# Performance work log

Measured on AMD Instinct MI355X. Metric: run time of the kernel, lower is better.

Reference implementation:

```python
import jax, jax.numpy as jnp
import numpy as np

HIDDEN = 2048
N_HEADS = 16
N_KV_HEADS = 4
HEAD_DIM = HIDDEN // N_HEADS  # 128
N_GROUPS = N_HEADS // N_KV_HEADS  # 4
ROPE_BASE = 10000.0


def rope_cos_sin(seq_len, dim, dtype=jnp.float32):
    inv_freq = 1.0 / (ROPE_BASE ** (jnp.arange(0, dim, 2, dtype=jnp.float32) / dim))
    t = jnp.arange(seq_len, dtype=jnp.float32)
    freqs = jnp.einsum('i,j->ij', t, inv_freq)          # [S, dim/2]
    emb = jnp.concatenate([freqs, freqs], axis=-1)       # [S, dim]
    return emb.astype(dtype).cos(), emb.astype(dtype).sin() if False else (jnp.cos(emb).astype(dtype), jnp.sin(emb).astype(dtype))[1] and None or (jnp.cos(emb).astype(dtype), jnp.sin(emb).astype(dtype))


def _rope_tables(seq_len, dim):
    inv_freq = 1.0 / (ROPE_BASE ** (jnp.arange(0, dim, 2, dtype=jnp.float32) / dim))
    t = jnp.arange(seq_len, dtype=jnp.float32)
    freqs = jnp.einsum('i,j->ij', t, inv_freq)
    emb = jnp.concatenate([freqs, freqs], axis=-1)
    return jnp.cos(emb), jnp.sin(emb)  # each [S, dim]


def rotate_half(x):
    d = x.shape[-1] // 2
    return jnp.concatenate([-x[..., d:], x[..., :d]], axis=-1)


def setup_inputs() -> dict:
    key = jax.random.key(0)
    ks = jax.random.split(key, 5)
    B, S = 2, 2048
    std = 0.02
    return {
        'hidden_states': jax.random.normal(ks[0], (B, S, HIDDEN), jnp.float32),
        'wq': jax.random.normal(ks[1], (HIDDEN, N_HEADS * HEAD_DIM), jnp.float32) * std,
        'wk': jax.random.normal(ks[2], (HIDDEN, N_KV_HEADS * HEAD_DIM), jnp.float32) * std,
        'wv': jax.random.normal(ks[3], (HIDDEN, N_KV_HEADS * HEAD_DIM), jnp.float32) * std,
        'wo': jax.random.normal(ks[4], (HIDDEN, HIDDEN), jnp.float32) * std,
    }


def reference(hidden_states, wq, wk, wv, wo):
    B, S, _ = hidden_states.shape
    q = (hidden_states @ wq).reshape(B, S, N_HEADS, HEAD_DIM)       # [B,S,Hq,D]
    k = (hidden_states @ wk).reshape(B, S, N_KV_HEADS, HEAD_DIM)    # [B,S,Hk,D]
    v = (hidden_states @ wv).reshape(B, S, N_KV_HEADS, HEAD_DIM)

    cos, sin = _rope_tables(S, HEAD_DIM)                            # [S,D]
    cos = cos[None, :, None, :]
    sin = sin[None, :, None, :]
    q = q * cos + rotate_half(q) * sin
    k = k * cos + rotate_half(k) * sin

    # GQA: repeat KV heads so kv head h maps to query heads h*G..h*G+G-1
    # (matches einops repeat 'b h s d -> b (h g) s d')
    k = jnp.repeat(k, N_GROUPS, axis=2)                              # [B,S,Hq,D]
    v = jnp.repeat(v, N_GROUPS, axis=2)

    scale = 1.0 / jnp.sqrt(jnp.asarray(HEAD_DIM, q.dtype))
    scores = jnp.einsum('bqhd,bkhd->bhqk', q, k) * scale            # [B,H,S,S]
    causal = jnp.triu(jnp.full((S, S), -jnp.inf, dtype=scores.dtype), k=1)
    scores = scores + causal
    probs = jax.nn.softmax(scores.astype(jnp.float32), axis=-1).astype(q.dtype)
    out = jnp.einsum('bhqk,bkhd->bqhd', probs, v)                   # [B,S,H,D]
    out = out.reshape(B, S, HIDDEN)
    return out @ wo
```

## Files before the change

### kernel.cpp

```cpp
#include <hip/hip_runtime.h>

#define HIDDEN 2048
#define NH 16
#define NKV 4
#define HD 128
#define BATCH 2
#define SEQ 2048
#define MROWS (BATCH*SEQ)
#define NQKV (NH*HD + 2*NKV*HD)
#define KOFF (NH*HD)
#define VOFF (NH*HD + NKV*HD)

typedef unsigned short u16;
typedef unsigned int u32;
typedef __bf16 bf16_t;
typedef bf16_t bf16x8 __attribute__((ext_vector_type(8)));
typedef float f32x4 __attribute__((ext_vector_type(4)));
typedef u16 u16x8 __attribute__((ext_vector_type(8)));

__device__ __forceinline__ u16 f2bf(float f) {
  u32 u = __builtin_bit_cast(u32, f);
  u32 r = (u + 0x7FFFu + ((u >> 16) & 1u)) >> 16;
  return (u16)r;
}
__device__ __forceinline__ float bf2f(u16 h) {
  u32 u = ((u32)h) << 16;
  return __builtin_bit_cast(float, u);
}

__global__ void cast_f32_bf16(const float* __restrict__ in, u16* __restrict__ out, int n8) {
  int i = blockIdx.x * blockDim.x + threadIdx.x;
  if (i >= n8) return;
  const float4* p = (const float4*)in + (size_t)i * 2;
  float4 a = p[0], b = p[1];
  u16x8 o;
  o[0]=f2bf(a.x); o[1]=f2bf(a.y); o[2]=f2bf(a.z); o[3]=f2bf(a.w);
  o[4]=f2bf(b.x); o[5]=f2bf(b.y); o[6]=f2bf(b.z); o[7]=f2bf(b.w);
  *((u16x8*)out + i) = o;
}

__global__ void transpose_cast(const float* __restrict__ src, u16* __restrict__ dst, int K, int N) {
  __shared__ float tile[32][33];
  int k0 = blockIdx.y * 32, n0 = blockIdx.x * 32;
  int tx = threadIdx.x, ty = threadIdx.y;
  #pragma unroll
  for (int j = 0; j < 32; j += 8)
    tile[ty + j][tx] = src[(size_t)(k0 + ty + j) * N + n0 + tx];
  __syncthreads();
  #pragma unroll
  for (int j = 0; j < 32; j += 8)
    dst[(size_t)(n0 + ty + j) * K + k0 + tx] = f2bf(tile[tx][ty + j]);
}

template<int OUT_BF16>
__global__ __launch_bounds__(256) void gemm_bt(const u16* __restrict__ A, const u16* __restrict__ Bt,
                                               void* __restrict__ Cout, int M, int N, int K) {
  __shared__ u16 As[2][128 * 32];
  __shared__ u16 Bs[2][128 * 32];
  const int tid = threadIdx.x;
  const int lane = tid & 63, wave = tid >> 6;
  const int mb = blockIdx.y * 128, nb = blockIdx.x * 128;
  const int wm = (wave >> 1) * 64, wn = (wave & 1) * 64;
  const int KT = K >> 5;

  auto stage = [&](int buf, int kt) {
    #pragma unroll
    for (int j = 0; j < 2; ++j) {
      int id0 = j * 256 + wave * 64;
      int id = id0 + lane;
      int row = id >> 2, c8 = (id & 3) * 8;
      const u16* ga = A + (size_t)(mb + row) * K + kt * 32 + c8;
      __builtin_amdgcn_global_load_lds((const __attribute__((address_space(1))) u32*)ga,
          (__attribute__((address_space(3))) u32*)&As[buf][id0 * 8], 16, 0, 0);
      const u16* gb = Bt + (size_t)(nb + row) * K + kt * 32 + c8;
      __builtin_amdgcn_global_load_lds((const __attribute__((address_space(1))) u32*)gb,
          (__attribute__((address_space(3))) u32*)&Bs[buf][id0 * 8], 16, 0, 0);
    }
  };

  f32x4 acc[4][4];
  #pragma unroll
  for (int i = 0; i < 4; ++i)
    #pragma unroll
    for (int j = 0; j < 4; ++j) acc[i][j] = (f32x4)0.0f;

  stage(0, 0);
  __syncthreads();
  for (int kt = 0; kt < KT; ++kt) {
    int cur = kt & 1;
    if (kt + 1 < KT) stage(cur ^ 1, kt + 1);
    bf16x8 af[4], bfr[4];
    #pragma unroll
    for (int mi = 0; mi < 4; ++mi) {
      int r = wm + mi * 16 + (lane & 15);
      af[mi] = __builtin_bit_cast(bf16x8, *(const u16x8*)&As[cur][r * 32 + (lane >> 4) * 8]);
    }
    #pragma unroll
    for (int ni = 0; ni < 4; ++ni) {
      int r = wn + ni * 16 + (lane & 15);
      bfr[ni] = __builtin_bit_cast(bf16x8, *(const u16x8*)&Bs[cur][r * 32 + (lane >> 4) * 8]);
    }
    #pragma unroll
    for (int mi = 0; mi < 4; ++mi)
      #pragma unroll
      for (int ni = 0; ni < 4; ++ni)
        acc[mi][ni] = __builtin_amdgcn_mfma_f32_16x16x32_bf16(af[mi], bfr[ni], acc[mi][ni], 0, 0, 0);
    __syncthreads();
  }
  int rbase = mb + wm + (lane >> 4) * 4;
  int cbase = nb + wn + (lane & 15);
  #pragma unroll
  for (int mi = 0; mi < 4; ++mi) {
    #pragma unroll
    for (int r = 0; r < 4; ++r) {
      int row = rbase + mi * 16 + r;
      #pragma unroll
      for (int ni = 0; ni < 4; ++ni) {
        int col = cbase + ni * 16;
        float v = acc[mi][ni][r];
        if (OUT_BF16) ((u16*)Cout)[(size_t)row * N + col] = f2bf(v);
        else          ((float*)Cout)[(size_t)row * N + col] = v;
      }
    }
  }
}

__global__ void rope_kernel(u16* __restrict__ qkv) {
  int idx = blockIdx.x * blockDim.x + threadIdx.x;
  int d = idx & 63;
  int t = idx >> 6;
  int hd = t % 20;
  int row = t / 20;
  int s = row & (SEQ - 1);
  int cb = (hd < NH) ? hd * HD : KOFF + (hd - NH) * HD;
  float inv = __expf((float)d * -0.14391156f);
  float freq = (float)s * inv;
  float sn = sinf(freq), cs = cosf(freq);
  size_t base = (size_t)row * NQKV + cb + d;
  float x0 = bf2f(qkv[base]), x1 = bf2f(qkv[base + 64]);
  qkv[base]      = f2bf(x0 * cs - x1 * sn);
  qkv[base + 64] = f2bf(x1 * cs + x0 * sn);
}

__global__ void vtrans_kernel(const u16* __restrict__ qkv, u16* __restrict__ vt) {
  __shared__ u16 tile[32][33];
  int bh = blockIdx.z;
  int d0 = blockIdx.y * 32;
  int s0 = blockIdx.x * 32;
  int b = bh >> 2, kvh = bh & 3;
  int tx = threadIdx.x, ty = threadIdx.y;
  const u16* src = qkv + (size_t)(b * SEQ) * NQKV + VOFF + kvh * HD;
  #pragma unroll
  for (int j = 0; j < 32; j += 8)
    tile[ty + j][tx] = src[(size_t)(s0 + ty + j) * NQKV + d0 + tx];
  __syncthreads();
  u16* dst = vt + (size_t)bh * HD * SEQ;
  #pragma unroll
  for (int j = 0; j < 32; j += 8)
    dst[(size_t)(d0 + ty + j) * SEQ + s0 + tx] = tile[tx][ty + j];
}

__global__ __launch_bounds__(512) void attn_kernel(const u16* __restrict__ qkv,
                                                   const u16* __restrict__ vt,
                                                   u16* __restrict__ out) {
  __shared__ u16 Ks[2][64 * 128];
  __shared__ u16 Vs[2][128 * 64];
  __shared__ u16 Ps[8][16 * 64];
  const int tid = threadIdx.x, lane = tid & 63, wave = tid >> 6;
  const int qtA = blockIdx.x, qtB = 15 - qtA;
  const int h = blockIdx.y, b = blockIdx.z;
  const int kvh = h >> 2;
  const int q0A = qtA * 128 + wave * 16;
  const int q0B = qtB * 128 + wave * 16;
  const float scale = 0.08838834764831845f;

  const u16* kbase = qkv + (size_t)(b * SEQ) * NQKV + KOFF + kvh * HD;
  const u16* vbase = vt + (size_t)(b * NKV + kvh) * HD * SEQ;

  bf16x8 qfA[4], qfB[4];
  {
    const u16* qa = qkv + (size_t)(b * SEQ + q0A + (lane & 15)) * NQKV + h * HD + (lane >> 4) * 8;
    const u16* qb = qkv + (size_t)(b * SEQ + q0B + (lane & 15)) * NQKV + h * HD + (lane >> 4) * 8;
    #pragma unroll
    for (int kc = 0; kc < 4; ++kc) {
      qfA[kc] = __builtin_bit_cast(bf16x8, *(const u16x8*)(qa + kc * 32));
      qfB[kc] = __builtin_bit_cast(bf16x8, *(const u16x8*)(qb + kc * 32));
    }
  }
  f32x4 oaccA[8], oaccB[8];
  float mA[4], lA[4], mB[4], lB[4];
  #pragma unroll
  for (int i = 0; i < 8; ++i) { oaccA[i] = (f32x4)0.0f; oaccB[i] = (f32x4)0.0f; }
  #pragma unroll
  for (int r = 0; r < 4; ++r) { mA[r] = -INFINITY; lA[r] = 0.0f; mB[r] = -INFINITY; lB[r] = 0.0f; }

  auto stage = [&](int buf, int t) {
    int kv0 = t * 64;
    #pragma unroll
    for (int j = 0; j < 2; ++j) {
      int kvr = wave * 8 + j * 4 + (lane >> 4);
      int sc = (lane & 15) ^ (kvr & 7);
      const u16* src = kbase + (size_t)(kv0 + kvr) * NQKV + sc * 8;
      __builtin_amdgcn_global_load_lds((const __attribute__((address_space(1))) u32*)src,
          (__attribute__((address_space(3))) u32*)&Ks[buf][(wave * 8 + j * 4) * 128], 16, 0, 0);
    }
    #pragma unroll
    for (int j = 0; j < 2; ++j) {
      int d = wave * 16 + j * 8 + (lane >> 3);
      int sc = (lane & 7) ^ (d & 7);
      const u16* src = vbase + (size_t)d * SEQ + kv0 + sc * 8;
      __builtin_amdgcn_global_load_lds((const __attribute__((address_space(1))) u32*)src,
          (__attribute__((address_space(3))) u32*)&Vs[buf][(wave * 16 + j * 8) * 64], 16, 0, 0);
    }
  };

  auto do_ctx = [&](const bf16x8 (&qf)[4], f32x4 (&oacc)[8], float (&mr)[4], float (&lr)[4],
                    int q0c, int kv0, int cur) {
    f32x4 sacc[4];
    #pragma unroll
    for (int n2 = 0; n2 < 4; ++n2) sacc[n2] = (f32x4)0.0f;
    #pragma unroll
    for (int n2 = 0; n2 < 4; ++n2) {
      int kvr = n2 * 16 + (lane & 15);
      #pragma unroll
      for (int kc = 0; kc < 4; ++kc) {
        int ch = (kc * 4 + (lane >> 4)) ^ (kvr & 7);
        bf16x8 kf = __builtin_bit_cast(bf16x8, *(const u16x8*)&Ks[cur][kvr * 128 + ch * 8]);
        sacc[n2] = __builtin_amdgcn_mfma_f32_16x16x32_bf16(qf[kc], kf, sacc[n2], 0, 0, 0);
      }
    }
    u16* pwb = &Ps[wave][0];
    #pragma unroll
    for (int r = 0; r < 4; ++r) {
      int qr = (lane >> 4) * 4 + r;
      int q = q0c + qr;
      float p0, p1, p2, p3;
      {
        int kvc = kv0 + (lane & 15);
        p0 = (kvc       <= q) ? sacc[0][r] * scale : -INFINITY;
        p1 = (kvc + 16  <= q) ? sacc[1][r] * scale : -INFINITY;
        p2 = (kvc + 32  <= q) ? sacc[2][r] * scale : -INFINITY;
        p3 = (kvc + 48  <= q) ? sacc[3][r] * scale : -INFINITY;
      }
      float v = fmaxf(fmaxf(p0, p1), fmaxf(p2, p3));
      v = fmaxf(v, __shfl_xor(v, 1));
      v = fmaxf(v, __shfl_xor(v, 2));
      v = fmaxf(v, __shfl_xor(v, 4));
      v = fmaxf(v, __shfl_xor(v, 8));
      float m = mr[r];
      if (v > m + 8.0f) {
        float corr = __expf(m - v);
        lr[r] *= corr;
        #pragma unroll
        for (int nt = 0; nt < 8; ++nt) oacc[nt][r] *= corr;
        m = v; mr[r] = v;
      }
      float e0 = __expf(p0 - m), e1 = __expf(p1 - m);
      float e2 = __expf(p2 - m), e3 = __expf(p3 - m);
      float ps = (e0 + e1) + (e2 + e3);
      ps += __shfl_xor(ps, 1);
      ps += __shfl_xor(ps, 2);
      ps += __shfl_xor(ps, 4);
      ps += __shfl_xor(ps, 8);
      lr[r] += ps;
      char* base = (char*)pwb + qr * 128 + (lane & 7) * 2;
      int half = (lane & 15) >> 3;
      *(u16*)(base + (((0 + half) ^ (qr & 7)) << 4)) = f2bf(e0);
      *(u16*)(base + (((2 + half) ^ (qr & 7)) << 4)) = f2bf(e1);
      *(u16*)(base + (((4 + half) ^ (qr & 7)) << 4)) = f2bf(e2);
      *(u16*)(base + (((6 + half) ^ (qr & 7)) << 4)) = f2bf(e3);
    }
    asm volatile("s_waitcnt lgkmcnt(0)" ::: "memory");
    bf16x8 pf[2];
    #pragma unroll
    for (int k2 = 0; k2 < 2; ++k2) {
      int q = lane & 15;
      int ch = (k2 * 4 + (lane >> 4)) ^ (q & 7);
      pf[k2] = __builtin_bit_cast(bf16x8, *(const u16x8*)((const char*)pwb + q * 128 + ch * 16));
    }
    #pragma unroll
    for (int nt = 0; nt < 8; ++nt) {
      int d = nt * 16 + (lane & 15);
      #pragma unroll
      for (int k2 = 0; k2 < 2; ++k2) {
        int ch = (k2 * 4 + (lane >> 4)) ^ (d & 7);
        bf16x8 vf = __builtin_bit_cast(bf16x8, *(const u16x8*)&Vs[cur][d * 64 + ch * 8]);
        oacc[nt] = __builtin_amdgcn_mfma_f32_16x16x32_bf16(pf[k2], vf, oacc[nt], 0, 0, 0);
      }
    }
  };

  const int nt_tiles = (qtB + 1) * 2;
  stage(0, 0);
  __syncthreads();
  for (int t = 0; t < nt_tiles; ++t) {
    int cur = t & 1;
    if (t + 1 < nt_tiles) stage(cur ^ 1, t + 1);
    int kv0 = t * 64;
    if (kv0 <= q0A + 15) do_ctx(qfA, oaccA, mA, lA, q0A, kv0, cur);
    if (kv0 <= q0B + 15) do_ctx(qfB, oaccB, mB, lB, q0B, kv0, cur);
    __syncthreads();
  }
  #pragma unroll
  for (int nt = 0; nt < 8; ++nt) {
    #pragma unroll
    for (int r = 0; r < 4; ++r) {
      int col = h * HD + nt * 16 + (lane & 15);
      int rowA = b * SEQ + q0A + (lane >> 4) * 4 + r;
      int rowB = b * SEQ + q0B + (lane >> 4) * 4 + r;
      out[(size_t)rowA * HIDDEN + col] = f2bf(oaccA[nt][r] / lA[r]);
      out[(size_t)rowB * HIDDEN + col] = f2bf(oaccB[nt][r] / lB[r]);
    }
  }
}

extern "C" void kernel_launch(void* const* d_in, const int* in_sizes, int n_in,
                              void* d_out, int out_size, void* d_ws, size_t ws_size,
                              hipStream_t stream) {
  (void)in_sizes; (void)n_in; (void)out_size; (void)ws_size;
  const float* x  = (const float*)d_in[0];
  const float* wq = (const float*)d_in[1];
  const float* wk = (const float*)d_in[2];
  const float* wv = (const float*)d_in[3];
  const float* wo = (const float*)d_in[4];
  float* out = (float*)d_out;
  char* ws = (char*)d_ws;

  u16* xbf   = (u16*)(ws);
  u16* wqkvt = (u16*)(ws + (size_t)16777216);
  u16* wot   = (u16*)(ws + (size_t)16777216 + 12582912);
  u16* qkv   = (u16*)(ws + (size_t)16777216 + 12582912 + 8388608);
  u16* vtb   = (u16*)(ws + (size_t)16777216 + 12582912 + 8388608 + 25165824);
  u16* aout  = xbf;

  cast_f32_bf16<<<4096, 256, 0, stream>>>(x, xbf, MROWS * HIDDEN / 8);
  transpose_cast<<<dim3(64, 64), dim3(32, 8), 0, stream>>>(wq, wqkvt, HIDDEN, 2048);
  transpose_cast<<<dim3(16, 64), dim3(32, 8), 0, stream>>>(wk, wqkvt + (size_t)2048 * 2048, HIDDEN, 512);
  transpose_cast<<<dim3(16, 64), dim3(32, 8), 0, stream>>>(wv, wqkvt + (size_t)2560 * 2048, HIDDEN, 512);
  transpose_cast<<<dim3(64, 64), dim3(32, 8), 0, stream>>>(wo, wot, HIDDEN, HIDDEN);

  gemm_bt<1><<<dim3(NQKV / 128, MROWS / 128), 256, 0, stream>>>(xbf, wqkvt, qkv, MROWS, NQKV, HIDDEN);
  rope_kernel<<<(MROWS * 20 * 64) / 256, 256, 0, stream>>>(qkv);
  vtrans_kernel<<<dim3(SEQ / 32, HD / 32, BATCH * NKV), dim3(32, 8), 0, stream>>>(qkv, vtb);
  attn_kernel<<<dim3(8, NH, BATCH), 512, 0, stream>>>(qkv, vtb, aout);
  gemm_bt<0><<<dim3(HIDDEN / 128, MROWS / 128), 256, 0, stream>>>(aout, wot, out, MROWS, HIDDEN, HIDDEN);
}
```

Baseline: 375.5 us.

## Use 256x256 GEMM tiles with swizzled LDS and retile attention to 64-row blocks

Replaces the 128x128 GEMM with a 256x256x64 tile kernel using 512 threads, XOR-swizzled LDS staging, interleaved fragment reloads and s_setprio around the MFMA groups. The attention kernel moves to 256-thread blocks handling 64-row query tiles, which doubles the grid. It also skips masking on fully unmasked tiles, switches the softmax to exp2 with a pre-folded log2e scale, and multiplies by a reciprocal in the epilogue. The float-to-bf16 conversion now uses the native cast. The larger GEMM tiles raise data reuse per block but produce fewer blocks (e.g. 16x12 for QKV) and a larger shared-memory footprint.

New measurement: 387.1 us. 1.03x slower.

```diff
diff --git a/kernel.cpp b/kernel.cpp
--- a/kernel.cpp
+++ b/kernel.cpp
@@ -19,9 +19,7 @@
 typedef u16 u16x8 __attribute__((ext_vector_type(8)));
 
 __device__ __forceinline__ u16 f2bf(float f) {
-  u32 u = __builtin_bit_cast(u32, f);
-  u32 r = (u + 0x7FFFu + ((u >> 16) & 1u)) >> 16;
-  return (u16)r;
+  return __builtin_bit_cast(u16, (__bf16)f);
 }
 __device__ __forceinline__ float bf2f(u16 h) {
   u32 u = ((u32)h) << 16;
@@ -53,64 +51,124 @@
 }
 
 template<int OUT_BF16>
-__global__ __launch_bounds__(256) void gemm_bt(const u16* __restrict__ A, const u16* __restrict__ Bt,
-                                               void* __restrict__ Cout, int M, int N, int K) {
-  __shared__ u16 As[2][128 * 32];
-  __shared__ u16 Bs[2][128 * 32];
+__global__ __launch_bounds__(512, 2) void gemm256(const u16* __restrict__ A, const u16* __restrict__ Bt,
+                                                  void* __restrict__ Cout, int M, int N, int K) {
+  __shared__ u16 As[2][256 * 64];
+  __shared__ u16 Bs[2][256 * 64];
   const int tid = threadIdx.x;
   const int lane = tid & 63, wave = tid >> 6;
-  const int mb = blockIdx.y * 128, nb = blockIdx.x * 128;
-  const int wm = (wave >> 1) * 64, wn = (wave & 1) * 64;
-  const int KT = K >> 5;
+  const int mb = blockIdx.y * 256, nb = blockIdx.x * 256;
+  const int wm = (wave >> 2) * 128;
+  const int wn = (wave & 3) * 64;
+  const int NT = K >> 6;
+
+  const int rsub = tid >> 3;
+  const int scol = (tid & 7) ^ (rsub & 7);
+  const int wbase = (tid & ~63);
 
   auto stage = [&](int buf, int kt) {
     #pragma unroll
-    for (int j = 0; j < 2; ++j) {
-      int id0 = j * 256 + wave * 64;
-      int id = id0 + lane;
-      int row = id >> 2, c8 = (id & 3) * 8;
-      const u16* ga = A + (size_t)(mb + row) * K + kt * 32 + c8;
+    for (int j = 0; j < 4; ++j) {
+      int r = j * 64 + rsub;
+      const u16* ga = A + (size_t)(mb + r) * K + kt * 64 + scol * 8;
       __builtin_amdgcn_global_load_lds((const __attribute__((address_space(1))) u32*)ga,
-          (__attribute__((address_space(3))) u32*)&As[buf][id0 * 8], 16, 0, 0);
-      const u16* gb = Bt + (size_t)(nb + row) * K + kt * 32 + c8;
+          (__attribute__((address_space(3))) u32*)&As[buf][(j * 512 + wbase) * 8], 16, 0, 0);
+      const u16* gb = Bt + (size_t)(nb + r) * K + kt * 64 + scol * 8;
       __builtin_amdgcn_global_load_lds((const __attribute__((address_space(1))) u32*)gb,
-          (__attribute__((address_space(3))) u32*)&Bs[buf][id0 * 8], 16, 0, 0);
+          (__attribute__((address_space(3))) u32*)&Bs[buf][(j * 512 + wbase) * 8], 16, 0, 0);
     }
   };
 
-  f32x4 acc[4][4];
-  #pragma unroll
-  for (int i = 0; i < 4; ++i)
+  f32x4 acc[8][4];
+  #pragma unroll
+  for (int i = 0; i < 8; ++i)
     #pragma unroll
     for (int j = 0; j < 4; ++j) acc[i][j] = (f32x4)0.0f;
+
+  const int arow = (lane & 15) * 64;
+  const int axor = lane & 7;
+  const int asel = lane >> 4;
 
   stage(0, 0);
   __syncthreads();
-  for (int kt = 0; kt < KT; ++kt) {
-    int cur = kt & 1;
-    if (kt + 1 < KT) stage(cur ^ 1, kt + 1);
-    bf16x8 af[4], bfr[4];
-    #pragma unroll
-    for (int mi = 0; mi < 4; ++mi) {
-      int r = wm + mi * 16 + (lane & 15);
-      af[mi] = __builtin_bit_cast(bf16x8, *(const u16x8*)&As[cur][r * 32 + (lane >> 4) * 8]);
-    }
-    #pragma unroll
-    for (int ni = 0; ni < 4; ++ni) {
-      int r = wn + ni * 16 + (lane & 15);
-      bfr[ni] = __builtin_bit_cast(bf16x8, *(const u16x8*)&Bs[cur][r * 32 + (lane >> 4) * 8]);
-    }
-    #pragma unroll
-    for (int mi = 0; mi < 4; ++mi)
-      #pragma unroll
-      for (int ni = 0; ni < 4; ++ni)
-        acc[mi][ni] = __builtin_amdgcn_mfma_f32_16x16x32_bf16(af[mi], bfr[ni], acc[mi][ni], 0, 0, 0);
+  for (int i = 0; i < NT; ++i) {
+    int cur = i & 1;
+    if (i + 1 < NT) stage(cur ^ 1, i + 1);
+
+    bf16x8 af[4][2], bfr[2][2];
+    #pragma unroll
+    for (int mi = 0; mi < 4; ++mi)
+      #pragma unroll
+      for (int ks = 0; ks < 2; ++ks)
+        af[mi][ks] = __builtin_bit_cast(bf16x8,
+          *(const u16x8*)&As[cur][(wm + mi * 16) * 64 + arow + (((ks * 4 + asel)) ^ axor) * 8]);
+    #pragma unroll
+    for (int ni = 0; ni < 2; ++ni)
+      #pragma unroll
+      for (int ks = 0; ks < 2; ++ks)
+        bfr[ni][ks] = __builtin_bit_cast(bf16x8,
+          *(const u16x8*)&Bs[cur][(wn + ni * 16) * 64 + arow + (((ks * 4 + asel)) ^ axor) * 8]);
+    __builtin_amdgcn_s_setprio(1);
+    #pragma unroll
+    for (int mi = 0; mi < 4; ++mi)
+      #pragma unroll
+      for (int ni = 0; ni < 2; ++ni)
+        #pragma unroll
+        for (int ks = 0; ks < 2; ++ks)
+          acc[mi][ni] = __builtin_amdgcn_mfma_f32_16x16x32_bf16(af[mi][ks], bfr[ni][ks], acc[mi][ni], 0, 0, 0);
+    __builtin_amdgcn_s_setprio(0);
+    #pragma unroll
+    for (int ni = 0; ni < 2; ++ni)
+      #pragma unroll
+      for (int ks = 0; ks < 2; ++ks)
+        bfr[ni][ks] = __builtin_bit_cast(bf16x8,
+          *(const u16x8*)&Bs[cur][(wn + (2 + ni) * 16) * 64 + arow + (((ks * 4 + asel)) ^ axor) * 8]);
+    __builtin_amdgcn_s_setprio(1);
+    #pragma unroll
+    for (int mi = 0; mi < 4; ++mi)
+      #pragma unroll
+      for (int ni = 0; ni < 2; ++ni)
+        #pragma unroll
+        for (int ks = 0; ks < 2; ++ks)
+          acc[mi][2 + ni] = __builtin_amdgcn_mfma_f32_16x16x32_bf16(af[mi][ks], bfr[ni][ks], acc[mi][2 + ni], 0, 0, 0);
+    __builtin_amdgcn_s_setprio(0);
+    #pragma unroll
+    for (int mi = 0; mi < 4; ++mi)
+      #pragma unroll
+      for (int ks = 0; ks < 2; ++ks)
+        af[mi][ks] = __builtin_bit_cast(bf16x8,
+          *(const u16x8*)&As[cur][(wm + (4 + mi) * 16) * 64 + arow + (((ks * 4 + asel)) ^ axor) * 8]);
+    __builtin_amdgcn_s_setprio(1);
+    #pragma unroll
+    for (int mi = 0; mi < 4; ++mi)
+      #pragma unroll
+      for (int ni = 0; ni < 2; ++ni)
+        #pragma unroll
+        for (int ks = 0; ks < 2; ++ks)
+          acc[4 + mi][2 + ni] = __builtin_amdgcn_mfma_f32_16x16x32_bf16(af[mi][ks], bfr[ni][ks], acc[4 + mi][2 + ni], 0, 0, 0);
+    __builtin_amdgcn_s_setprio(0);
+    #pragma unroll
+    for (int ni = 0; ni < 2; ++ni)
+      #pragma unroll
+      for (int ks = 0; ks < 2; ++ks)
+        bfr[ni][ks] = __builtin_bit_cast(bf16x8,
+          *(const u16x8*)&Bs[cur][(wn + ni * 16) * 64 + arow + (((ks * 4 + asel)) ^ axor) * 8]);
+    __builtin_amdgcn_s_setprio(1);
+    #pragma unroll
+    for (int mi = 0; mi < 4; ++mi)
+      #pragma unroll
+      for (int ni = 0; ni < 2; ++ni)
+        #pragma unroll
+        for (int ks = 0; ks < 2; ++ks)
+          acc[4 + mi][ni] = __builtin_amdgcn_mfma_f32_16x16x32_bf16(af[mi][ks], bfr[ni][ks], acc[4 + mi][ni], 0, 0, 0);
+    __builtin_amdgcn_s_setprio(0);
+
     __syncthreads();
   }
   int rbase = mb + wm + (lane >> 4) * 4;
   int cbase = nb + wn + (lane & 15);
   #pragma unroll
-  for (int mi = 0; mi < 4; ++mi) {
+  for (int mi = 0; mi < 8; ++mi) {
     #pragma unroll
     for (int r = 0; r < 4; ++r) {
       int row = rbase + mi * 16 + r;
@@ -160,19 +218,19 @@
     dst[(size_t)(d0 + ty + j) * SEQ + s0 + tx] = tile[tx][ty + j];
 }
 
-__global__ __launch_bounds__(512) void attn_kernel(const u16* __restrict__ qkv,
-                                                   const u16* __restrict__ vt,
-                                                   u16* __restrict__ out) {
+__global__ __launch_bounds__(256, 2) void attn_kernel(const u16* __restrict__ qkv,
+                                                      const u16* __restrict__ vt,
+                                                      u16* __restrict__ out) {
   __shared__ u16 Ks[2][64 * 128];
   __shared__ u16 Vs[2][128 * 64];
-  __shared__ u16 Ps[8][16 * 64];
+  __shared__ u16 Ps[4][16 * 64];
   const int tid = threadIdx.x, lane = tid & 63, wave = tid >> 6;
-  const int qtA = blockIdx.x, qtB = 15 - qtA;
+  const int qtA = blockIdx.x, qtB = 31 - qtA;
   const int h = blockIdx.y, b = blockIdx.z;
   const int kvh = h >> 2;
-  const int q0A = qtA * 128 + wave * 16;
-  const int q0B = qtB * 128 + wave * 16;
-  const float scale = 0.08838834764831845f;
+  const int q0A = qtA * 64 + wave * 16;
+  const int q0B = qtB * 64 + wave * 16;
+  const float scale2 = 0.12751743f;
 
   const u16* kbase = qkv + (size_t)(b * SEQ) * NQKV + KOFF + kvh * HD;
   const u16* vbase = vt + (size_t)(b * NKV + kvh) * HD * SEQ;
@@ -194,23 +252,25 @@
   #pragma unroll
   for (int r = 0; r < 4; ++r) { mA[r] = -INFINITY; lA[r] = 0.0f; mB[r] = -INFINITY; lB[r] = 0.0f; }
 
+  const int krow = tid >> 4;
+  const int kslot = (tid & 15) ^ (krow & 7);
+  const int vrow = tid >> 3;
+  const int vslot = (tid & 7) ^ (vrow & 7);
+  const int wbase = (tid & ~63);
+
   auto stage = [&](int buf, int t) {
     int kv0 = t * 64;
     #pragma unroll
-    for (int j = 0; j < 2; ++j) {
-      int kvr = wave * 8 + j * 4 + (lane >> 4);
-      int sc = (lane & 15) ^ (kvr & 7);
-      const u16* src = kbase + (size_t)(kv0 + kvr) * NQKV + sc * 8;
+    for (int j = 0; j < 4; ++j) {
+      const u16* src = kbase + (size_t)(kv0 + j * 16 + krow) * NQKV + kslot * 8;
       __builtin_amdgcn_global_load_lds((const __attribute__((address_space(1))) u32*)src,
-          (__attribute__((address_space(3))) u32*)&Ks[buf][(wave * 8 + j * 4) * 128], 16, 0, 0);
-    }
-    #pragma unroll
-    for (int j = 0; j < 2; ++j) {
-      int d = wave * 16 + j * 8 + (lane >> 3);
-      int sc = (lane & 7) ^ (d & 7);
-      const u16* src = vbase + (size_t)d * SEQ + kv0 + sc * 8;
+          (__attribute__((address_space(3))) u32*)&Ks[buf][(j * 256 + wbase) * 8], 16, 0, 0);
+    }
+    #pragma unroll
+    for (int j = 0; j < 4; ++j) {
+      const u16* src = vbase + (size_t)(j * 32 + vrow) * SEQ + kv0 + vslot * 8;
       __builtin_amdgcn_global_load_lds((const __attribute__((address_space(1))) u32*)src,
-          (__attribute__((address_space(3))) u32*)&Vs[buf][(wave * 16 + j * 8) * 64], 16, 0, 0);
+          (__attribute__((address_space(3))) u32*)&Vs[buf][(j * 256 + wbase) * 8], 16, 0, 0);
     }
   };
 
@@ -229,18 +289,22 @@
         sacc[n2] = __builtin_amdgcn_mfma_f32_16x16x32_bf16(qf[kc], kf, sacc[n2], 0, 0, 0);
       }
     }
+    const bool full = (kv0 + 63 <= q0c);
     u16* pwb = &Ps[wave][0];
     #pragma unroll
     for (int r = 0; r < 4; ++r) {
       int qr = (lane >> 4) * 4 + r;
-      int q = q0c + qr;
       float p0, p1, p2, p3;
-      {
+      if (full) {
+        p0 = sacc[0][r] * scale2; p1 = sacc[1][r] * scale2;
+        p2 = sacc[2][r] * scale2; p3 = sacc[3][r] * scale2;
+      } else {
+        int q = q0c + qr;
         int kvc = kv0 + (lane & 15);
-        p0 = (kvc       <= q) ? sacc[0][r] * scale : -INFINITY;
-        p1 = (kvc + 16  <= q) ? sacc[1][r] * scale : -INFINITY;
-        p2 = (kvc + 32  <= q) ? sacc[2][r] * scale : -INFINITY;
-        p3 = (kvc + 48  <= q) ? sacc[3][r] * scale : -INFINITY;
+        p0 = (kvc       <= q) ? sacc[0][r] * scale2 : -INFINITY;
+        p1 = (kvc + 16  <= q) ? sacc[1][r] * scale2 : -INFINITY;
+        p2 = (kvc + 32  <= q) ? sacc[2][r] * scale2 : -INFINITY;
+        p3 = (kvc + 48  <= q) ? sacc[3][r] * scale2 : -INFINITY;
       }
       float v = fmaxf(fmaxf(p0, p1), fmaxf(p2, p3));
       v = fmaxf(v, __shfl_xor(v, 1));
@@ -249,14 +313,14 @@
       v = fmaxf(v, __shfl_xor(v, 8));
       float m = mr[r];
       if (v > m + 8.0f) {
-        float corr = __expf(m - v);
+        float corr = exp2f(m - v);
         lr[r] *= corr;
         #pragma unroll
         for (int nt = 0; nt < 8; ++nt) oacc[nt][r] *= corr;
         m = v; mr[r] = v;
       }
-      float e0 = __expf(p0 - m), e1 = __expf(p1 - m);
-      float e2 = __expf(p2 - m), e3 = __expf(p3 - m);
+      float e0 = exp2f(p0 - m), e1 = exp2f(p1 - m);
+      float e2 = exp2f(p2 - m), e3 = exp2f(p3 - m);
       float ps = (e0 + e1) + (e2 + e3);
       ps += __shfl_xor(ps, 1);
       ps += __shfl_xor(ps, 2);
@@ -290,7 +354,7 @@
     }
   };
 
-  const int nt_tiles = (qtB + 1) * 2;
+  const int nt_tiles = qtB + 1;
   stage(0, 0);
   __syncthreads();
   for (int t = 0; t < nt_tiles; ++t) {
@@ -302,14 +366,15 @@
     __syncthreads();
   }
   #pragma unroll
-  for (int nt = 0; nt < 8; ++nt) {
-    #pragma unroll
-    for (int r = 0; r < 4; ++r) {
+  for (int r = 0; r < 4; ++r) {
+    float invA = 1.0f / lA[r], invB = 1.0f / lB[r];
+    #pragma unroll
+    for (int nt = 0; nt < 8; ++nt) {
       int col = h * HD + nt * 16 + (lane & 15);
       int rowA = b * SEQ + q0A + (lane >> 4) * 4 + r;
       int rowB = b * SEQ + q0B + (lane >> 4) * 4 + r;
-      out[(size_t)rowA * HIDDEN + col] = f2bf(oaccA[nt][r] / lA[r]);
-      out[(size_t)rowB * HIDDEN + col] = f2bf(oaccB[nt][r] / lB[r]);
+      out[(size_t)rowA * HIDDEN + col] = f2bf(oaccA[nt][r] * invA);
+      out[(size_t)rowB * HIDDEN + col] = f2bf(oaccB[nt][r] * invB);
     }
   }
 }
@@ -339,9 +404,9 @@
   transpose_cast<<<dim3(16, 64), dim3(32, 8), 0, stream>>>(wv, wqkvt + (size_t)2560 * 2048, HIDDEN, 512);
   transpose_cast<<<dim3(64, 64), dim3(32, 8), 0, stream>>>(wo, wot, HIDDEN, HIDDEN);
 
-  gemm_bt<1><<<dim3(NQKV / 128, MROWS / 128), 256, 0, stream>>>(xbf, wqkvt, qkv, MROWS, NQKV, HIDDEN);
+  gemm256<1><<<dim3(NQKV / 256, MROWS / 256), 512, 0, stream>>>(xbf, wqkvt, qkv, MROWS, NQKV, HIDDEN);
   rope_kernel<<<(MROWS * 20 * 64) / 256, 256, 0, stream>>>(qkv);
   vtrans_kernel<<<dim3(SEQ / 32, HD / 32, BATCH * NKV), dim3(32, 8), 0, stream>>>(qkv, vtb);
-  attn_kernel<<<dim3(8, NH, BATCH), 512, 0, stream>>>(qkv, vtb, aout);
-  gemm_bt<0><<<dim3(HIDDEN / 128, MROWS / 128), 256, 0, stream>>>(aout, wot, out, MROWS, HIDDEN, HIDDEN);
-}
+  attn_kernel<<<dim3(16, NH, BATCH), 256, 0, stream>>>(qkv, vtb, aout);
+  gemm256<0><<<dim3(HIDDEN / 256, MROWS / 256), 512, 0, stream>>>(aout, wot, out, MROWS, HIDDEN, HIDDEN);
+}
```
